# Performance work log

Measured on AMD Instinct MI355X. Metric: run time of the kernel, lower is better.

The kernel has to match this reference:

```python
import jax, jax.numpy as jnp
import numpy as np

N, D, K, NCB = 65536, 256, 1024, 4


def setup_inputs() -> dict:
    key = jax.random.key(0)
    kz, kc = jax.random.split(key)
    z = jax.random.normal(kz, (N, D), dtype=jnp.float32)
    # nn.Embedding weights init: uniform(-1/k, 1/k)
    codebooks = jax.random.uniform(kc, (NCB, K, D), dtype=jnp.float32,
                                   minval=-1.0 / K, maxval=1.0 / K)
    return {"z": z, "codebooks": codebooks}


def _vq_step(r, W):
    """One VQ codebook pass. r: [N, D], W: [k, D].
    Squared L2 distance via matmul trick: ||r||^2 - 2 r.W^T + ||W||^2,
    same math as sum((r[:,None,:]-W)**2, -1) without the [N,k,D] blowup."""
    r2 = jnp.sum(r * r, axis=-1, keepdims=True)            # [N, 1]
    w2 = jnp.sum(W * W, axis=-1)                           # [k]
    dist = r2 - 2.0 * (r @ W.T) + w2                       # [N, k]
    ind = jnp.argmin(dist, axis=-1)                        # [N]
    z_q = W[ind]                                           # [N, D]
    sg = jax.lax.stop_gradient
    vq_loss = jnp.mean((z_q - sg(r)) ** 2)
    commitment_loss = jnp.mean((r - sg(z_q)) ** 2)
    z_q_st = r + sg(z_q - r)                               # straight-through
    return z_q_st, ind, vq_loss + commitment_loss


def reference(z, codebooks):
    residual = z
    quant_sum = jnp.zeros_like(z)
    inds = []
    total_loss = jnp.zeros((), dtype=z.dtype)
    for i in range(codebooks.shape[0]):  # small fixed loop over codebooks
        z_q, ind, loss = _vq_step(residual, codebooks[i])
        residual = residual - z_q
        quant_sum = quant_sum + z_q
        inds.append(ind)
        total_loss = total_loss + loss
    return quant_sum, jnp.stack(inds, axis=1), total_loss
```

## Files before the change

kernel.cpp:

```cpp
#include <hip/hip_runtime.h>


#define N_TOK 65536
#define DIM   256
#define KCB   1024
#define NCBK  4

#define TM  32
#define TK  256
#define DC  32
#define RST 260

#define QS_F   ((size_t)N_TOK * DIM)
#define IDX_F  QS_F
#define IDXE_F (IDX_F + (size_t)N_TOK * NCBK)
#define LOSS_F IDXE_F

#define WS_PART_OFF 16384
#define WS_FLAG_OFF 32768

typedef unsigned short u16;
typedef unsigned int   u32;

__device__ __forceinline__ float bf2f(u32 h) { return __uint_as_float(h << 16); }

__device__ __forceinline__ float getv(const void* base, int f32in, size_t elt) {
    if (f32in) return ((const float*)base)[elt];
    return bf2f(((const u16*)base)[elt]);
}

__device__ __forceinline__ void load8(const void* base, int f32in, size_t elt,
                                      float* f) {
    if (f32in) {
        const float4* p = (const float4*)((const float*)base + elt);
        float4 a = p[0], b = p[1];
        f[0] = a.x; f[1] = a.y; f[2] = a.z; f[3] = a.w;
        f[4] = b.x; f[5] = b.y; f[6] = b.z; f[7] = b.w;
    } else {
        uint4 q = *(const uint4*)((const u16*)base + elt);
        f[0] = bf2f(q.x & 0xffffu); f[1] = bf2f(q.x >> 16);
        f[2] = bf2f(q.y & 0xffffu); f[3] = bf2f(q.y >> 16);
        f[4] = bf2f(q.z & 0xffffu); f[5] = bf2f(q.z >> 16);
        f[6] = bf2f(q.w & 0xffffu); f[7] = bf2f(q.w >> 16);
    }
}

__global__ void canary_kernel(float* out) {
    int gid = blockIdx.x * 256 + threadIdx.x;
    size_t pos = IDX_F + (size_t)gid;
    if (pos < IDXE_F) out[pos] = 512.0f;
    if (gid == 0) out[LOSS_F] = 512.0f;
}

__global__ void detect_kernel(const u16* z16, const u16* cb16, int* flags) {
    __shared__ int s0[256], s1[256];
    int tid = threadIdx.x;
    u32 a = z16[tid],  ea = (a >> 7) & 0xffu;
    u32 b = cb16[tid], eb = (b >> 7) & 0xffu;
    s0[tid] = ((ea >= 90u && ea <= 140u) || ((a & 0x7fffu) == 0u)) ? 1 : 0;
    s1[tid] = ((eb >= 90u && eb <= 140u) || ((b & 0x7fffu) == 0u)) ? 1 : 0;
    __syncthreads();
    for (int st = 128; st > 0; st >>= 1) {
        if (tid < st) { s0[tid] += s0[tid + st]; s1[tid] += s1[tid + st]; }
        __syncthreads();
    }
    if (tid == 0) { flags[0] = (s0[0] < 218) ? 1 : 0;
                    flags[1] = (s1[0] < 218) ? 1 : 0; }
}

__device__ __forceinline__ float np128_sq_g(const void* base, int f32in, size_t off) {
    float S[16];
    #pragma unroll
    for (int l = 0; l < 16; ++l) {
        float A[8];
        #pragma unroll
        for (int j = 0; j < 8; ++j) {
            float x = getv(base, f32in, off + 16 * j + l);
            A[j] = x * x;
        }
        S[l] = ((A[0] + A[1]) + (A[2] + A[3])) + ((A[4] + A[5]) + (A[6] + A[7]));
    }
    float B1[8], B2[4];
    #pragma unroll
    for (int l = 0; l < 8; ++l) B1[l] = S[l] + S[l + 8];
    #pragma unroll
    for (int l = 0; l < 4; ++l) B2[l] = B1[l] + B1[l + 4];
    return (B2[0] + B2[2]) + (B2[1] + B2[3]);
}

__device__ __forceinline__ float np128_sq_lds(const float* a) {
    float S[16];
    #pragma unroll
    for (int l = 0; l < 16; ++l) {
        float A[8];
        #pragma unroll
        for (int j = 0; j < 8; ++j) { float x = a[16 * j + l]; A[j] = x * x; }
        S[l] = ((A[0] + A[1]) + (A[2] + A[3])) + ((A[4] + A[5]) + (A[6] + A[7]));
    }
    float B1[8], B2[4];
    #pragma unroll
    for (int l = 0; l < 8; ++l) B1[l] = S[l] + S[l + 8];
    #pragma unroll
    for (int l = 0; l < 4; ++l) B2[l] = B1[l] + B1[l + 4];
    return (B2[0] + B2[2]) + (B2[1] + B2[3]);
}

__global__ void w2_kernel(const void* cbs, float* w2f, const int* flags) {
    int kf = blockIdx.x * 256 + threadIdx.x;
    const int fc = flags[1];
    size_t base = (size_t)kf * DIM;
    w2f[kf] = np128_sq_g(cbs, fc, base) + np128_sq_g(cbs, fc, base + 128);
}

__global__ __launch_bounds__(256, 2)
void rq_kernel(const void* z, const void* cbs, const float* w2f,
               float* out, double* partials, const int* flags) {
    __shared__ float  Rld[TM * RST];
    __shared__ float  Wld[512 * 16];
    __shared__ float  candv[TM * 33];
    __shared__ int    candi[TM * 33];
    __shared__ float  r2s[TM];
    __shared__ int    bestk[TM];
    __shared__ double dred[256];

    const int fz = flags[0], fc = flags[1];
    const int tid  = threadIdx.x;
    const int tx   = tid & 31;
    const int ty   = tid >> 5;
    const int row0 = blockIdx.x * TM;

    const int K2 = ((tx >> 1) & 7) << 2;

    float q[32];
    #pragma unroll
    for (int e = 0; e < 32; ++e) q[e] = 0.f;

    for (int it = 0; it < 4; ++it) {
        int flat = it * 256 + tid;
        int r = flat >> 5, c8 = flat & 31;
        float f[8];
        load8(z, fz, (size_t)(row0 + r) * DIM + c8 * 8, f);
        int base = r * RST + c8 * 8;
        #pragma unroll
        for (int e = 0; e < 8; ++e) Rld[base + e] = f[e];
    }
    double lsum = 0.0;

    for (int cb = 0; cb < NCBK; ++cb) {
        const size_t cbW = (size_t)cb * KCB * DIM;
        const float* w2c = w2f + cb * KCB;

        __syncthreads();
        if (tid < TM) {
            const float* a = &Rld[tid * RST];
            r2s[tid] = np128_sq_lds(a) + np128_sq_lds(a + 128);
        }
        __syncthreads();

        float r2v[4];
        #pragma unroll
        for (int i = 0; i < 4; ++i) r2v[i] = r2s[ty + 8 * i];

        float bval[4]; int bidx[4];
        #pragma unroll
        for (int i = 0; i < 4; ++i) { bval[i] = __uint_as_float(0x7f7fffffu); bidx[i] = 0; }

        for (int kt = 0; kt < KCB / TK; ++kt) {
            float acc[4][8];
            #pragma unroll
            for (int i = 0; i < 4; ++i)
                #pragma unroll
                for (int j = 0; j < 8; ++j) acc[i][j] = 0.f;

            for (int dc = 0; dc < DIM / DC; ++dc) {
                __syncthreads();
                #pragma unroll
                for (int it = 0; it < 4; ++it) {
                    int k  = it * 64 + (tid >> 2);
                    int dp = (tid & 3) * 8;
                    float f[8];
                    load8(cbs, fc, cbW + (size_t)(kt * TK + k) * DIM + dc * DC + dp, f);
                    int row = k + ((dp >> 4) << 8);
                    int kw2 = ((k >> 1) & 7) << 2;
                    int g0  = (dp & 15) >> 2;
                    int fi0 = ((row << 4) + (g0 << 2)) ^ kw2;
                    int fi1 = ((row << 4) + ((g0 + 1) << 2)) ^ kw2;
                    *(float4*)&Wld[fi0] = make_float4(f[0], f[1], f[2], f[3]);
                    *(float4*)&Wld[fi1] = make_float4(f[4], f[5], f[6], f[7]);
                }
                __syncthreads();

                #pragma unroll
                for (int dd = 0; dd < DC / 4; ++dd) {
                    float4 av[4];
                    #pragma unroll
                    for (int i = 0; i < 4; ++i)
                        av[i] = *(const float4*)
                            &Rld[(ty + 8 * i) * RST + dc * DC + dd * 4];
                    const int tb = ((dd >> 2) << 12) + ((dd & 3) << 2);
                    #pragma unroll
                    for (int j = 0; j < 8; ++j) {
                        const int fi = (((tx + 32 * j) << 4) + tb) ^ K2;
                        const float4 bv = *(const float4*)&Wld[fi];
                        #pragma unroll
                        for (int i = 0; i < 4; ++i) {
                            float s = acc[i][j];
                            s = fmaf(av[i].x, bv.x, s);
                            s = fmaf(av[i].y, bv.y, s);
                            s = fmaf(av[i].z, bv.z, s);
                            s = fmaf(av[i].w, bv.w, s);
                            acc[i][j] = s;
                        }
                    }
                }
            }
            #pragma unroll
            for (int j = 0; j < 8; ++j) {
                int k = kt * TK + tx + 32 * j;
                float w2k = w2c[k];
                #pragma unroll
                for (int i = 0; i < 4; ++i) {
                    float t2   = r2v[i] - 2.0f * acc[i][j];
                    float dist = t2 + w2k;
                    if (dist < bval[i] || (dist == bval[i] && k < bidx[i])) {
                        bval[i] = dist; bidx[i] = k;
                    }
                }
            }
        }
        __syncthreads();
        #pragma unroll
        for (int i = 0; i < 4; ++i) {
            int r = ty + 8 * i;
            candv[r * 33 + tx] = bval[i];
            candi[r * 33 + tx] = bidx[i];
        }
        __syncthreads();
        if (tid < TM) {
            float best = candv[tid * 33];
            int   bi   = candi[tid * 33];
            for (int t = 1; t < 32; ++t) {
                float v = candv[tid * 33 + t];
                int  ix = candi[tid * 33 + t];
                if (v < best || (v == best && ix < bi)) { best = v; bi = ix; }
            }
            bestk[tid] = bi;
            size_t pos = IDX_F + (size_t)(row0 + tid) * NCBK + cb;
            if (pos < IDXE_F) out[pos] = (float)bi;
        }
        __syncthreads();
        #pragma unroll
        for (int it = 0; it < 4; ++it) {
            int flat = it * 256 + tid;
            int r = flat >> 5, c8 = flat & 31;
            int kb = bestk[r];
            float f[8];
            load8(cbs, fc, cbW + (size_t)kb * DIM + c8 * 8, f);
            int base = r * RST + c8 * 8;
            #pragma unroll
            for (int e = 0; e < 8; ++e) {
                float rv = Rld[base + e];
                float t  = f[e] - rv;
                float s  = rv + t;
                float rn = rv - s;
                Rld[base + e] = rn;
                q[it * 8 + e] = q[it * 8 + e] + s;
                lsum += (double)t * (double)t;
            }
        }
        __syncthreads();
    }

    #pragma unroll
    for (int it = 0; it < 4; ++it) {
        int flat = it * 256 + tid;
        int r = flat >> 5, c8 = flat & 31;
        size_t pos = (size_t)(row0 + r) * DIM + c8 * 8;
        if (pos + 8 <= QS_F) {
            #pragma unroll
            for (int e = 0; e < 8; ++e) out[pos + e] = q[it * 8 + e];
        }
    }

    dred[tid] = lsum;
    __syncthreads();
    for (int s = 128; s > 0; s >>= 1) {
        if (tid < s) dred[tid] += dred[tid + s];
        __syncthreads();
    }
    if (tid == 0) partials[blockIdx.x] = dred[0];
}

__global__ void loss_final(const double* partials, float* out) {
    __shared__ double sred[256];
    int tid = threadIdx.x;
    double s = 0.0;
    for (int q = 0; q < 8; ++q) s += partials[tid + 256 * q];
    sred[tid] = s;
    __syncthreads();
    for (int st = 128; st > 0; st >>= 1) {
        if (tid < st) sred[tid] += sred[tid + st];
        __syncthreads();
    }
    if (tid == 0)
        out[LOSS_F] = (float)(2.0 * sred[0] / 16777216.0);
}

extern "C" void kernel_launch(void* const* d_in, const int* in_sizes, int n_in,
                              void* d_out, int out_size, void* d_ws, size_t ws_size,
                              hipStream_t stream) {
    (void)n_in; (void)out_size; (void)ws_size;
    const void* z;
    const void* cbs;
    if (in_sizes[0] == 16777216) { z = d_in[0]; cbs = d_in[1]; }
    else                         { z = d_in[1]; cbs = d_in[0]; }

    float*  out      = (float*)d_out;
    float*  w2f      = (float*)d_ws;
    double* partials = (double*)((char*)d_ws + WS_PART_OFF);
    int*    flags    = (int*)((char*)d_ws + WS_FLAG_OFF);

    canary_kernel<<<1024, 256, 0, stream>>>(out);
    detect_kernel<<<1, 256, 0, stream>>>((const u16*)z, (const u16*)cbs, flags);
    w2_kernel<<<16, 256, 0, stream>>>(cbs, w2f, flags);
    rq_kernel<<<N_TOK / TM, 256, 0, stream>>>(z, cbs, w2f, out, partials, flags);
    loss_final<<<1, 256, 0, stream>>>(partials, out);
}
```

Baseline: 2.660 ms.

## Shrink codebook LDS tile and alias scratch buffers to fit three blocks per CU

Halves the d-chunk staged per iteration (DC 32→16) and replaces the XOR-swizzled float4 codebook tile with a padded row layout (stride 18) read as float2 pairs. The candidate, index and reduction scratch arrays now alias the codebook tile instead of having their own storage, which cuts LDS use so launch bounds can request three blocks per CU. The goal is higher occupancy to hide load latency. In exchange it doubles the number of barriers per k-tile, moves from 128-bit to 64-bit LDS reads, and may add register pressure under the tighter launch bound.

```diff
diff --git a/kernel.cpp b/kernel.cpp
--- a/kernel.cpp
+++ b/kernel.cpp
@@ -8,8 +8,9 @@
 
 #define TM  32
 #define TK  256
-#define DC  32
+#define DC  16
 #define RST 260
+#define WST 18
 
 #define QS_F   ((size_t)N_TOK * DIM)
 #define IDX_F  QS_F
@@ -112,16 +113,17 @@
     w2f[kf] = np128_sq_g(cbs, fc, base) + np128_sq_g(cbs, fc, base + 128);
 }
 
-__global__ __launch_bounds__(256, 2)
+__global__ __launch_bounds__(256, 3)
 void rq_kernel(const void* z, const void* cbs, const float* w2f,
                float* out, double* partials, const int* flags) {
     __shared__ float  Rld[TM * RST];
-    __shared__ float  Wld[512 * 16];
-    __shared__ float  candv[TM * 33];
-    __shared__ int    candi[TM * 33];
+    __shared__ __align__(16) float Wld[TK * WST];
     __shared__ float  r2s[TM];
     __shared__ int    bestk[TM];
-    __shared__ double dred[256];
+
+    float*  candv = Wld;
+    int*    candi = (int*)(Wld + TM * 33);
+    double* dred  = (double*)Wld;
 
     const int fz = flags[0], fc = flags[1];
     const int tid  = threadIdx.x;
@@ -129,7 +131,8 @@
     const int ty   = tid >> 5;
     const int row0 = blockIdx.x * TM;
 
-    const int K2 = ((tx >> 1) & 7) << 2;
+    const int stg_k0 = tid >> 1;
+    const int stg_dp = (tid & 1) * 8;
 
     float q[32];
     #pragma unroll
@@ -175,18 +178,15 @@
             for (int dc = 0; dc < DIM / DC; ++dc) {
                 __syncthreads();
                 #pragma unroll
-                for (int it = 0; it < 4; ++it) {
-                    int k  = it * 64 + (tid >> 2);
-                    int dp = (tid & 3) * 8;
+                for (int it = 0; it < 2; ++it) {
+                    int k = it * 128 + stg_k0;
                     float f[8];
-                    load8(cbs, fc, cbW + (size_t)(kt * TK + k) * DIM + dc * DC + dp, f);
-                    int row = k + ((dp >> 4) << 8);
-                    int kw2 = ((k >> 1) & 7) << 2;
-                    int g0  = (dp & 15) >> 2;
-                    int fi0 = ((row << 4) + (g0 << 2)) ^ kw2;
-                    int fi1 = ((row << 4) + ((g0 + 1) << 2)) ^ kw2;
-                    *(float4*)&Wld[fi0] = make_float4(f[0], f[1], f[2], f[3]);
-                    *(float4*)&Wld[fi1] = make_float4(f[4], f[5], f[6], f[7]);
+                    load8(cbs, fc, cbW + (size_t)(kt * TK + k) * DIM + dc * DC + stg_dp, f);
+                    int wb = k * WST + stg_dp;
+                    *(float2*)&Wld[wb]     = make_float2(f[0], f[1]);
+                    *(float2*)&Wld[wb + 2] = make_float2(f[2], f[3]);
+                    *(float2*)&Wld[wb + 4] = make_float2(f[4], f[5]);
+                    *(float2*)&Wld[wb + 6] = make_float2(f[6], f[7]);
                 }
                 __syncthreads();
 
@@ -197,18 +197,19 @@
                     for (int i = 0; i < 4; ++i)
                         av[i] = *(const float4*)
                             &Rld[(ty + 8 * i) * RST + dc * DC + dd * 4];
-                    const int tb = ((dd >> 2) << 12) + ((dd & 3) << 2);
                     #pragma unroll
                     for (int j = 0; j < 8; ++j) {
-                        const int fi = (((tx + 32 * j) << 4) + tb) ^ K2;
-                        const float4 bv = *(const float4*)&Wld[fi];
+                        const int c = tx + 32 * j;
+                        const float2* wp = (const float2*)&Wld[c * WST + dd * 4];
+                        const float2 b01 = wp[0];
+                        const float2 b23 = wp[1];
                         #pragma unroll
                         for (int i = 0; i < 4; ++i) {
                             float s = acc[i][j];
-                            s = fmaf(av[i].x, bv.x, s);
-                            s = fmaf(av[i].y, bv.y, s);
-                            s = fmaf(av[i].z, bv.z, s);
-                            s = fmaf(av[i].w, bv.w, s);
+                            s = fmaf(av[i].x, b01.x, s);
+                            s = fmaf(av[i].y, b01.y, s);
+                            s = fmaf(av[i].z, b23.x, s);
+                            s = fmaf(av[i].w, b23.y, s);
                             acc[i][j] = s;
                         }
                     }
```

After: 2.809 ms. 5.6% more time.
